# Kernel optimization log

Measured on AMD Instinct MI355X. Metric: run time of the kernel, lower is better.

## Reference

```python
import jax, jax.numpy as jnp
import numpy as np

N_NODES = 50000
N_FEAT = 128
N_EDGES = 1600000
HID = 64


def gcn_conv(x, row, col, w, W, b, n):
    """PyG GCNConv with edge weights and added self-loops (fill_value=1).
    x: [N, Fin]; row/col: [E] (src, dst); w: [E]; W: [Fin, Fout]; b: [Fout].
    """
    loop = jnp.arange(n)
    r = jnp.concatenate([row, loop])
    c = jnp.concatenate([col, loop])
    ww = jnp.concatenate([w, jnp.ones((n,), dtype=x.dtype)])
    deg = jax.ops.segment_sum(ww, c, num_segments=n)  # [N]
    dinv = jnp.where(deg > 0, jax.lax.rsqrt(deg), 0.0)
    norm = dinv[r] * ww * dinv[c]  # [E+N]
    xw = x @ W  # [N, Fout] -- linear before propagate, as in PyG
    msg = norm[:, None] * xw[r]  # gather + scale
    out = jax.ops.segment_sum(msg, c, num_segments=n)  # scatter-add
    return out + b


def setup_inputs() -> dict:
    key = jax.random.key(0)
    ks = jax.random.split(key, 12)
    features = jax.random.normal(ks[0], (N_NODES, N_FEAT), dtype=jnp.float32)
    edge_index = jax.random.randint(ks[1], (2, N_EDGES), 0, N_NODES, dtype=jnp.int64)
    edge_attr = jax.random.uniform(ks[2], (N_EDGES,), dtype=jnp.float32)
    s = 0.05
    # generator encoder: GCNConv(n_feat->64), GCNConv(64->n_feat)
    Wg1 = jax.random.normal(ks[3], (N_FEAT, HID), dtype=jnp.float32) * s
    bg1 = jnp.zeros((HID,), dtype=jnp.float32)
    Wg2 = jax.random.normal(ks[4], (HID, N_FEAT), dtype=jnp.float32) * s
    bg2 = jnp.zeros((N_FEAT,), dtype=jnp.float32)
    # discriminator: GCNConv(n_feat->64), Linear(n_nodes*64 -> 1)
    Wd1 = jax.random.normal(ks[5], (N_FEAT, HID), dtype=jnp.float32) * s
    bd1 = jnp.zeros((HID,), dtype=jnp.float32)
    wfc = jax.random.normal(ks[6], (N_NODES * HID,), dtype=jnp.float32) * 0.001
    bfc = jnp.zeros((), dtype=jnp.float32)
    return {"features": features, "edge_index": edge_index, "edge_attr": edge_attr,
            "Wg1": Wg1, "bg1": bg1, "Wg2": Wg2, "bg2": bg2,
            "Wd1": Wd1, "bd1": bd1, "wfc": wfc, "bfc": bfc}


def reference(features, edge_index, edge_attr, Wg1, bg1, Wg2, bg2, Wd1, bd1, wfc, bfc):
    n = features.shape[0]
    row, col = edge_index[0], edge_index[1]
    # --- generator encoder (eval mode: dropout is a no-op) ---
    h = gcn_conv(features, row, col, edge_attr, Wg1, bg1, n)
    h = jax.nn.relu(h)
    z = jax.nn.sigmoid(gcn_conv(h, row, col, edge_attr, Wg2, bg2, n))  # [N, n_feat]
    # --- GAE inner-product decoder over the given edge list ---
    edge_probs = jax.nn.sigmoid(jnp.sum(z[row] * z[col], axis=-1))  # [E]
    # residual connection
    enc = z + features
    edge_probs = jnp.nan_to_num(edge_probs, nan=0.0)
    # --- discriminator (eval mode: no noise, no dropout) ---
    d = gcn_conv(enc, row, col, edge_probs, Wd1, bd1, n)
    d = jax.nn.relu(d)
    logit = jnp.dot(d.reshape(-1), wfc) + bfc
    return jax.nn.sigmoid(logit)
```

## Files before the change

### kernel.cpp

```cpp
#include <hip/hip_runtime.h>
#include <math.h>

static constexpr int NN = 50000;
static constexpr int NF = 128;
static constexpr int NH = 64;
static constexpr int NE = 1600000;
static constexpr int NBUSED = (NN + 255) / 256;
static constexpr int NWG = 256;
static constexpr int CHUNK = NE / NWG;

typedef unsigned long long u64;
typedef float f32x2 __attribute__((ext_vector_type(2)));


__device__ __forceinline__ float bf2f(unsigned u) { return __uint_as_float(u << 16); }
__device__ __forceinline__ unsigned short f2bf(float f) {
  unsigned b = __float_as_uint(f);
  b += 0x7fffu + ((b >> 16) & 1u);
  return (unsigned short)(b >> 16);
}
__device__ __forceinline__ float sigm(float x) { return 1.f / (1.f + __expf(-x)); }
__device__ __forceinline__ unsigned char f2fp8(float f) {
  int v = __builtin_amdgcn_cvt_pk_fp8_f32(f, f, 0, false);
  return (unsigned char)(v & 0xff);
}
__device__ __forceinline__ void fp8x16_dec(uint4 v, float* o) {
  f32x2 t;
  t = __builtin_amdgcn_cvt_pk_f32_fp8(v.x, false); o[0] = t.x;  o[1] = t.y;
  t = __builtin_amdgcn_cvt_pk_f32_fp8(v.x, true);  o[2] = t.x;  o[3] = t.y;
  t = __builtin_amdgcn_cvt_pk_f32_fp8(v.y, false); o[4] = t.x;  o[5] = t.y;
  t = __builtin_amdgcn_cvt_pk_f32_fp8(v.y, true);  o[6] = t.x;  o[7] = t.y;
  t = __builtin_amdgcn_cvt_pk_f32_fp8(v.z, false); o[8] = t.x;  o[9] = t.y;
  t = __builtin_amdgcn_cvt_pk_f32_fp8(v.z, true);  o[10] = t.x; o[11] = t.y;
  t = __builtin_amdgcn_cvt_pk_f32_fp8(v.w, false); o[12] = t.x; o[13] = t.y;
  t = __builtin_amdgcn_cvt_pk_f32_fp8(v.w, true);  o[14] = t.x; o[15] = t.y;
}
__device__ __forceinline__ uint4 fp8x16_enc(const float* o) {
  uint4 r;
  int v;
  v = __builtin_amdgcn_cvt_pk_fp8_f32(o[0], o[1], 0, false);
  v = __builtin_amdgcn_cvt_pk_fp8_f32(o[2], o[3], v, true);
  r.x = (unsigned)v;
  v = __builtin_amdgcn_cvt_pk_fp8_f32(o[4], o[5], 0, false);
  v = __builtin_amdgcn_cvt_pk_fp8_f32(o[6], o[7], v, true);
  r.y = (unsigned)v;
  v = __builtin_amdgcn_cvt_pk_fp8_f32(o[8], o[9], 0, false);
  v = __builtin_amdgcn_cvt_pk_fp8_f32(o[10], o[11], v, true);
  r.z = (unsigned)v;
  v = __builtin_amdgcn_cvt_pk_fp8_f32(o[12], o[13], 0, false);
  v = __builtin_amdgcn_cvt_pk_fp8_f32(o[14], o[15], v, true);
  r.w = (unsigned)v;
  return r;
}


__global__ __launch_bounds__(256) void bhist_k(const int* __restrict__ col,
                                               int* __restrict__ counts) {
  __shared__ int cnt[256];
  cnt[threadIdx.x] = 0;
  __syncthreads();
  int g = blockIdx.x;
  int e1 = g * CHUNK + CHUNK;
  for (int e = g * CHUNK + threadIdx.x; e < e1; e += 256)
    atomicAdd(&cnt[col[e] >> 8], 1);
  __syncthreads();
  counts[g * 256 + threadIdx.x] = cnt[threadIdx.x];
}

__global__ __launch_bounds__(256) void bscan_k(int* __restrict__ counts) {
  __shared__ int sm[256];
  int b = threadIdx.x;
  int tot = 0;
  for (int g = 0; g < NWG; g++) tot += counts[g * 256 + b];
  sm[b] = tot;
  __syncthreads();
  int v = tot;
  for (int off = 1; off < 256; off <<= 1) {
    int u = (b >= off) ? sm[b - off] : 0;
    __syncthreads();
    sm[b] += u;
    __syncthreads();
  }
  int run = sm[b] - v;
  for (int g = 0; g < NWG; g++) {
    int c = counts[g * 256 + b];
    counts[g * 256 + b] = run;
    run += c;
  }
}

__global__ __launch_bounds__(256) void bpart_k(const int* __restrict__ row,
                                               const int* __restrict__ col,
                                               const float* __restrict__ w,
                                               const int* __restrict__ counts,
                                               u64* __restrict__ ebuf) {
  __shared__ int cur[256];
  int g = blockIdx.x;
  cur[threadIdx.x] = counts[g * 256 + threadIdx.x];
  __syncthreads();
  int e1 = g * CHUNK + CHUNK;
  for (int e = g * CHUNK + threadIdx.x; e < e1; e += 256) {
    int c = col[e];
    int p = atomicAdd(&cur[c >> 8], 1);
    u64 pk = ((u64)(unsigned)__float_as_int(w[e]) << 32) |
             ((unsigned)(c & 255) << 16) | (unsigned)row[e];
    ebuf[p] = pk;
  }
}

__global__ __launch_bounds__(256) void bsortA_k(const u64* __restrict__ ebuf,
                                                const int* __restrict__ counts,
                                                int* __restrict__ rowstart,
                                                float* __restrict__ dinv) {
  __shared__ int cnt[256];
  __shared__ float deg[256];
  __shared__ int sm[256];
  int b = blockIdx.x, t = threadIdx.x;
  cnt[t] = 0;
  deg[t] = 1.0f;
  __syncthreads();
  int boff = counts[b];
  int bend = (b < NBUSED - 1) ? counts[b + 1] : NE;
  for (int e = boff + t; e < bend; e += 256) {
    u64 pk = ebuf[e];
    unsigned lo = (unsigned)pk;
    int c = (lo >> 16) & 255;
    atomicAdd(&cnt[c], 1);
    atomicAdd(&deg[c], __uint_as_float((unsigned)(pk >> 32)));
  }
  __syncthreads();
  int v = cnt[t];
  sm[t] = v;
  __syncthreads();
  for (int off = 1; off < 256; off <<= 1) {
    int u = (t >= off) ? sm[t - off] : 0;
    __syncthreads();
    sm[t] += u;
    __syncthreads();
  }
  int colg = b * 256 + t;
  if (colg < NN) {
    rowstart[colg] = boff + sm[t] - v;
    dinv[colg] = rsqrtf(deg[t]);
  }
  if (b == NBUSED - 1 && t == 0) rowstart[NN] = NE;
}

__global__ __launch_bounds__(256) void bsortB_k(const u64* __restrict__ ebuf,
                                                const int* __restrict__ counts,
                                                const int* __restrict__ rowstart,
                                                const float* __restrict__ dinv,
                                                unsigned* __restrict__ es4) {
  __shared__ int cur[256];
  int b = blockIdx.x, t = threadIdx.x;
  int colg = b * 256 + t;
  cur[t] = (colg < NN) ? rowstart[colg] : NE;
  __syncthreads();
  int boff = counts[b];
  int bend = (b < NBUSED - 1) ? counts[b + 1] : NE;
  for (int e = boff + t; e < bend; e += 256) {
    u64 pk = ebuf[e];
    unsigned lo = (unsigned)pk;
    int r = lo & 0xffff;
    int c = (lo >> 16) & 255;
    float wv = __uint_as_float((unsigned)(pk >> 32));
    int p = atomicAdd(&cur[c], 1);
    es4[p] = ((unsigned)f2bf(dinv[r] * wv) << 16) | (unsigned)r;
  }
}

template<int K, int M, int ACT, bool OUTF, bool OUTH, bool XH, bool OUT8>
__global__ __launch_bounds__(256) void gemm_k(const float* __restrict__ X,
                                              const unsigned short* __restrict__ Xh,
                                              const float* __restrict__ Xadd,
                                              const float* __restrict__ W,
                                              const float* __restrict__ bias,
                                              float* __restrict__ Yf,
                                              unsigned short* __restrict__ Yh,
                                              unsigned char* __restrict__ Y8) {
  __shared__ float Ws[K * M];
  __shared__ float Xs[16][K];
  for (int i = threadIdx.x; i < K * M; i += 256) Ws[i] = W[i];
  int r0 = blockIdx.x * 16;
  for (int i = threadIdx.x; i < 16 * K; i += 256) {
    int r = i / K, k = i % K;
    size_t off = (size_t)(r0 + r) * K + k;
    float v = XH ? bf2f(Xh[off]) : X[off];
    if (Xadd) v += Xadd[off];
    Xs[r][k] = v;
  }
  __syncthreads();
  constexpr int RPT = 16 * M / 256;
  constexpr int RS = 256 / M;
  int colc = threadIdx.x % M;
  int rb = threadIdx.x / M;
  float acc[RPT];
#pragma unroll
  for (int i = 0; i < RPT; i++) acc[i] = 0.f;
  for (int k = 0; k < K; k++) {
    float wv = Ws[k * M + colc];
#pragma unroll
    for (int i = 0; i < RPT; i++) acc[i] += Xs[rb + i * RS][k] * wv;
  }
#pragma unroll
  for (int i = 0; i < RPT; i++) {
    int r = r0 + rb + i * RS;
    float o = acc[i];
    if (ACT > 0) o += bias[colc];
    if (ACT == 2) o = sigm(o);
    if (OUTF) Yf[(size_t)r * M + colc] = o;
    if (OUTH) Yh[(size_t)r * M + colc] = f2bf(o);
    if (OUT8) Y8[(size_t)r * M + colc] = f2fp8(o);
  }
}

template<int MODE>
__global__ __launch_bounds__(256) void agg64_k(const int* __restrict__ rowstart,
                                               const unsigned* __restrict__ es4,
                                               const unsigned char* __restrict__ src8,
                                               const float* __restrict__ dinv,
                                               const float* __restrict__ bias,
                                               unsigned char* __restrict__ out8,
                                               unsigned short* __restrict__ outh,
                                               float* __restrict__ outf,
                                               const float* __restrict__ wfc) {
  int wid = (blockIdx.x * 256 + threadIdx.x) >> 6;
  int lane = threadIdx.x & 63;
  int sub = lane >> 2;
  int l = lane & 3;
  int e0 = rowstart[wid], e1 = rowstart[wid + 1];
  float di = dinv[wid];
  float a[16];
#pragma unroll
  for (int c = 0; c < 16; c++) a[c] = 0.f;
  for (int eb = e0; eb < e1; eb += 32) {
    int eA = eb + sub;
    int eB = eb + 16 + sub;
    bool vA = eA < e1, vB = eB < e1;
    unsigned erA = es4[vA ? eA : e0];
    unsigned erB = es4[vB ? eB : e0];
    int rA = (int)(erA & 0xffffu);
    int rB = (int)(erB & 0xffffu);
    float nmA, nmB;
    if (MODE == 2) {
      nmA = vA ? dinv[rA] * bf2f(erA >> 16) : 0.f;
      nmB = vB ? dinv[rB] * bf2f(erB >> 16) : 0.f;
    } else {
      nmA = vA ? bf2f(erA >> 16) : 0.f;
      nmB = vB ? bf2f(erB >> 16) : 0.f;
    }
    uint4 gA = *(const uint4*)(src8 + (size_t)rA * 64 + l * 16);
    uint4 gB = *(const uint4*)(src8 + (size_t)rB * 64 + l * 16);
    float tA[16], tB[16];
    fp8x16_dec(gA, tA);
    fp8x16_dec(gB, tB);
#pragma unroll
    for (int c = 0; c < 16; c++) a[c] = fmaf(nmA, tA[c], a[c]);
#pragma unroll
    for (int c = 0; c < 16; c++) a[c] = fmaf(nmB, tB[c], a[c]);
  }
#pragma unroll
  for (int c = 0; c < 16; c++) {
    a[c] += __shfl_xor(a[c], 4);
    a[c] += __shfl_xor(a[c], 8);
    a[c] += __shfl_xor(a[c], 16);
    a[c] += __shfl_xor(a[c], 32);
  }
  uint4 sv = *(const uint4*)(src8 + (size_t)wid * 64 + l * 16);
  float sf[16];
  fp8x16_dec(sv, sf);

  if (MODE == 0) {
    if (sub == 0) {
      float o[16];
#pragma unroll
      for (int c4 = 0; c4 < 4; c4++) {
        float4 b4 = *(const float4*)(bias + l * 16 + c4 * 4);
        o[c4 * 4 + 0] = fmaxf(di * (a[c4 * 4 + 0] + di * sf[c4 * 4 + 0]) + b4.x, 0.f);
        o[c4 * 4 + 1] = fmaxf(di * (a[c4 * 4 + 1] + di * sf[c4 * 4 + 1]) + b4.y, 0.f);
        o[c4 * 4 + 2] = fmaxf(di * (a[c4 * 4 + 2] + di * sf[c4 * 4 + 2]) + b4.z, 0.f);
        o[c4 * 4 + 3] = fmaxf(di * (a[c4 * 4 + 3] + di * sf[c4 * 4 + 3]) + b4.w, 0.f);
      }
      *(uint4*)(out8 + (size_t)wid * 64 + l * 16) = fp8x16_enc(o);
    }
  } else if (MODE == 1) {
    if (sub == 0) {
      float o[16];
#pragma unroll
      for (int c = 0; c < 16; c++) o[c] = di * (a[c] + di * sf[c]);
      uint4 p0, p1;
      p0.x = (unsigned)f2bf(o[0]) | ((unsigned)f2bf(o[1]) << 16);
      p0.y = (unsigned)f2bf(o[2]) | ((unsigned)f2bf(o[3]) << 16);
      p0.z = (unsigned)f2bf(o[4]) | ((unsigned)f2bf(o[5]) << 16);
      p0.w = (unsigned)f2bf(o[6]) | ((unsigned)f2bf(o[7]) << 16);
      p1.x = (unsigned)f2bf(o[8]) | ((unsigned)f2bf(o[9]) << 16);
      p1.y = (unsigned)f2bf(o[10]) | ((unsigned)f2bf(o[11]) << 16);
      p1.z = (unsigned)f2bf(o[12]) | ((unsigned)f2bf(o[13]) << 16);
      p1.w = (unsigned)f2bf(o[14]) | ((unsigned)f2bf(o[15]) << 16);
      *(uint4*)(outh + (size_t)wid * 64 + l * 16) = p0;
      *(uint4*)(outh + (size_t)wid * 64 + l * 16 + 8) = p1;
    }
  } else {
    float s = 0.f;
    if (sub == 0) {
#pragma unroll
      for (int c4 = 0; c4 < 4; c4++) {
        float4 b4 = *(const float4*)(bias + l * 16 + c4 * 4);
        float4 w4 = *(const float4*)(wfc + (size_t)wid * 64 + l * 16 + c4 * 4);
        float o0 = fmaxf(di * (a[c4 * 4 + 0] + di * sf[c4 * 4 + 0]) + b4.x, 0.f);
        float o1 = fmaxf(di * (a[c4 * 4 + 1] + di * sf[c4 * 4 + 1]) + b4.y, 0.f);
        float o2 = fmaxf(di * (a[c4 * 4 + 2] + di * sf[c4 * 4 + 2]) + b4.z, 0.f);
        float o3 = fmaxf(di * (a[c4 * 4 + 3] + di * sf[c4 * 4 + 3]) + b4.w, 0.f);
        s += o0 * w4.x + o1 * w4.y + o2 * w4.z + o3 * w4.w;
      }
    }
    s += __shfl_xor(s, 1);
    s += __shfl_xor(s, 2);
    __shared__ float bs[4];
    if (lane == 0) bs[threadIdx.x >> 6] = s;
    __syncthreads();
    if (threadIdx.x == 0) outf[blockIdx.x] = bs[0] + bs[1] + bs[2] + bs[3];
  }
}

__global__ __launch_bounds__(256) void eprob16_k(const int* __restrict__ rowstart,
                                                 unsigned* __restrict__ es4,
                                                 const unsigned char* __restrict__ z8,
                                                 float* __restrict__ dinv2) {
  int wid = (blockIdx.x * 256 + threadIdx.x) >> 6;
  int lane = threadIdx.x & 63;
  int sub = lane >> 3;
  int l = lane & 7;
  uint4 zv = *(const uint4*)(z8 + (size_t)wid * NF + l * 16);
  float zi[16];
  fp8x16_dec(zv, zi);
  int e0 = rowstart[wid], e1 = rowstart[wid + 1];
  float sum = 0.f;
  for (int eb = e0; eb < e1; eb += 16) {
    int eA = eb + sub;
    int eB = eb + 8 + sub;
    bool vA = eA < e1, vB = eB < e1;
    unsigned erA = es4[vA ? eA : e0];
    unsigned erB = es4[vB ? eB : e0];
    int rA = (int)(erA & 0xffffu);
    int rB = (int)(erB & 0xffffu);
    uint4 a4 = *(const uint4*)(z8 + (size_t)rA * NF + l * 16);
    uint4 b4 = *(const uint4*)(z8 + (size_t)rB * NF + l * 16);
    float zr[16];
    fp8x16_dec(a4, zr);
    float dA = 0.f;
#pragma unroll
    for (int c = 0; c < 16; c++) dA = fmaf(zr[c], zi[c], dA);
    fp8x16_dec(b4, zr);
    float dB = 0.f;
#pragma unroll
    for (int c = 0; c < 16; c++) dB = fmaf(zr[c], zi[c], dB);
    dA += __shfl_xor(dA, 1);
    dA += __shfl_xor(dA, 2);
    dA += __shfl_xor(dA, 4);
    dB += __shfl_xor(dB, 1);
    dB += __shfl_xor(dB, 2);
    dB += __shfl_xor(dB, 4);
    if (vA && l == 0) {
      float p = sigm(dA);
      es4[eA] = ((unsigned)f2bf(p) << 16) | (unsigned)rA;
      sum += p;
    }
    if (vB && l == 0) {
      float p = sigm(dB);
      es4[eB] = ((unsigned)f2bf(p) << 16) | (unsigned)rB;
      sum += p;
    }
  }
  sum += __shfl_xor(sum, 8);
  sum += __shfl_xor(sum, 16);
  sum += __shfl_xor(sum, 32);
  if (lane == 0) dinv2[wid] = rsqrtf(1.f + sum);
}

__global__ __launch_bounds__(256) void reduce_k(const float* __restrict__ partials, int n,
                                                const float* __restrict__ bfc,
                                                float* __restrict__ out) {
  float s = 0.f;
  for (int i = threadIdx.x; i < n; i += 256) s += partials[i];
  s += __shfl_xor(s, 1);
  s += __shfl_xor(s, 2);
  s += __shfl_xor(s, 4);
  s += __shfl_xor(s, 8);
  s += __shfl_xor(s, 16);
  s += __shfl_xor(s, 32);
  __shared__ float ws4[4];
  if ((threadIdx.x & 63) == 0) ws4[threadIdx.x >> 6] = s;
  __syncthreads();
  if (threadIdx.x == 0) out[0] = sigm(ws4[0] + ws4[1] + ws4[2] + ws4[3] + bfc[0]);
}


extern "C" void kernel_launch(void* const* d_in, const int* in_sizes, int n_in,
                              void* d_out, int out_size, void* d_ws, size_t ws_size,
                              hipStream_t stream) {
  const float* features = (const float*)d_in[0];
  const int* edge_index = (const int*)d_in[1];
  const float* edge_attr = (const float*)d_in[2];
  const float* Wg1 = (const float*)d_in[3];
  const float* bg1 = (const float*)d_in[4];
  const float* Wg2 = (const float*)d_in[5];
  const float* bg2 = (const float*)d_in[6];
  const float* Wd1 = (const float*)d_in[7];
  const float* bd1 = (const float*)d_in[8];
  const float* wfc = (const float*)d_in[9];
  const float* bfc = (const float*)d_in[10];
  float* out = (float*)d_out;

  const int* row = edge_index;
  const int* col = edge_index + NE;

  char* wsb = (char*)d_ws;
  auto carve = [&](size_t bytes) {
    void* p = wsb;
    wsb += (bytes + 255) & ~(size_t)255;
    return p;
  };
  int*   counts   = (int*)carve((size_t)NWG * 256 * 4);
  int*   rowstart = (int*)carve((NN + 1) * 4);
  float* dinv     = (float*)carve(NN * 4);
  float* dinv2    = (float*)carve(NN * 4);
  u64*   ebuf     = (u64*)carve((size_t)NE * 8);
  unsigned* es4   = (unsigned*)carve((size_t)NE * 4);
  unsigned char* xw8a = (unsigned char*)carve((size_t)NN * NH);
  unsigned char* hh8  = (unsigned char*)carve((size_t)NN * NH);
  unsigned short* ahh = (unsigned short*)carve((size_t)NN * NH * 2);
  unsigned short* zh = (unsigned short*)carve((size_t)NN * NF * 2);
  unsigned char* z8  = (unsigned char*)carve((size_t)NN * NF);
  unsigned char* xw8d = (unsigned char*)carve((size_t)NN * NH);
  float* partials = (float*)carve(12500 * 4);

  const int GG = NN / 16;
  const int GW = NN * 64 / 256;

  bhist_k<<<NWG, 256, 0, stream>>>(col, counts);
  bscan_k<<<1, 256, 0, stream>>>(counts);
  bpart_k<<<NWG, 256, 0, stream>>>(row, col, edge_attr, counts, ebuf);
  bsortA_k<<<NBUSED, 256, 0, stream>>>(ebuf, counts, rowstart, dinv);
  bsortB_k<<<NBUSED, 256, 0, stream>>>(ebuf, counts, rowstart, dinv, es4);

  gemm_k<NF, NH, 0, false, false, false, true><<<GG, 256, 0, stream>>>(
      features, nullptr, nullptr, Wg1, nullptr, nullptr, nullptr, xw8a);
  agg64_k<0><<<GW, 256, 0, stream>>>(rowstart, es4, xw8a, dinv, bg1, hh8, nullptr, nullptr,
                                     nullptr);

  agg64_k<1><<<GW, 256, 0, stream>>>(rowstart, es4, hh8, dinv, nullptr, nullptr, ahh, nullptr,
                                     nullptr);
  gemm_k<NH, NF, 2, false, true, true, true><<<GG, 256, 0, stream>>>(
      nullptr, ahh, nullptr, Wg2, bg2, nullptr, zh, z8);

  eprob16_k<<<GW, 256, 0, stream>>>(rowstart, es4, z8, dinv2);

  gemm_k<NF, NH, 0, false, false, true, true><<<GG, 256, 0, stream>>>(
      nullptr, zh, features, Wd1, nullptr, nullptr, nullptr, xw8d);
  agg64_k<2><<<GW, 256, 0, stream>>>(rowstart, es4, xw8d, dinv2, bd1, nullptr, nullptr,
                                     partials, wfc);

  reduce_k<<<1, 256, 0, stream>>>(partials, GW, bfc, out);
}
```

Baseline: 336.7 us.

## Fuse bucket sort passes and move source-degree scaling into aggregation; add nontemporal hints

Merges the two per-bucket sort kernels into one, so the bucket's ebuf slice is re-read while cached and one launch disappears. Since dinv is no longer ready when edges are written, the stored edge value becomes the raw weight and every aggregation mode multiplies by dinv[row] at gather time, which adds a dependent gather per edge. Nontemporal load/store hints are also added on the streaming edge arrays and the aggregation outputs to reduce cache pollution.

New measurement: 423.1 us. 1.26x slower.

```diff
diff --git a/kernel.cpp b/kernel.cpp
--- a/kernel.cpp
+++ b/kernel.cpp
@@ -11,6 +11,7 @@
 
 typedef unsigned long long u64;
 typedef float f32x2 __attribute__((ext_vector_type(2)));
+typedef unsigned u32x4 __attribute__((ext_vector_type(4)));
 
 
 __device__ __forceinline__ float bf2f(unsigned u) { return __uint_as_float(u << 16); }
@@ -35,8 +36,8 @@
   t = __builtin_amdgcn_cvt_pk_f32_fp8(v.w, false); o[12] = t.x; o[13] = t.y;
   t = __builtin_amdgcn_cvt_pk_f32_fp8(v.w, true);  o[14] = t.x; o[15] = t.y;
 }
-__device__ __forceinline__ uint4 fp8x16_enc(const float* o) {
-  uint4 r;
+__device__ __forceinline__ u32x4 fp8x16_enc(const float* o) {
+  u32x4 r;
   int v;
   v = __builtin_amdgcn_cvt_pk_fp8_f32(o[0], o[1], 0, false);
   v = __builtin_amdgcn_cvt_pk_fp8_f32(o[2], o[3], v, true);
@@ -62,7 +63,7 @@
   int g = blockIdx.x;
   int e1 = g * CHUNK + CHUNK;
   for (int e = g * CHUNK + threadIdx.x; e < e1; e += 256)
-    atomicAdd(&cnt[col[e] >> 8], 1);
+    atomicAdd(&cnt[__builtin_nontemporal_load(&col[e]) >> 8], 1);
   __syncthreads();
   counts[g * 256 + threadIdx.x] = cnt[threadIdx.x];
 }
@@ -100,21 +101,25 @@
   __syncthreads();
   int e1 = g * CHUNK + CHUNK;
   for (int e = g * CHUNK + threadIdx.x; e < e1; e += 256) {
-    int c = col[e];
+    int c = __builtin_nontemporal_load(&col[e]);
+    float wv = __builtin_nontemporal_load(&w[e]);
+    int r = __builtin_nontemporal_load(&row[e]);
     int p = atomicAdd(&cur[c >> 8], 1);
-    u64 pk = ((u64)(unsigned)__float_as_int(w[e]) << 32) |
-             ((unsigned)(c & 255) << 16) | (unsigned)row[e];
-    ebuf[p] = pk;
-  }
-}
-
-__global__ __launch_bounds__(256) void bsortA_k(const u64* __restrict__ ebuf,
-                                                const int* __restrict__ counts,
-                                                int* __restrict__ rowstart,
-                                                float* __restrict__ dinv) {
+    u64 pk = ((u64)(unsigned)__float_as_int(wv) << 32) |
+             ((unsigned)(c & 255) << 16) | (unsigned)r;
+    __builtin_nontemporal_store(pk, &ebuf[p]);
+  }
+}
+
+__global__ __launch_bounds__(256) void bsortAB_k(const u64* __restrict__ ebuf,
+                                                 const int* __restrict__ counts,
+                                                 int* __restrict__ rowstart,
+                                                 float* __restrict__ dinv,
+                                                 unsigned* __restrict__ es4) {
   __shared__ int cnt[256];
   __shared__ float deg[256];
   __shared__ int sm[256];
+  __shared__ int cur[256];
   int b = blockIdx.x, t = threadIdx.x;
   cnt[t] = 0;
   deg[t] = 1.0f;
@@ -138,34 +143,22 @@
     sm[t] += u;
     __syncthreads();
   }
+  int start = boff + sm[t] - v;
+  cur[t] = start;
   int colg = b * 256 + t;
   if (colg < NN) {
-    rowstart[colg] = boff + sm[t] - v;
+    rowstart[colg] = start;
     dinv[colg] = rsqrtf(deg[t]);
   }
   if (b == NBUSED - 1 && t == 0) rowstart[NN] = NE;
-}
-
-__global__ __launch_bounds__(256) void bsortB_k(const u64* __restrict__ ebuf,
-                                                const int* __restrict__ counts,
-                                                const int* __restrict__ rowstart,
-                                                const float* __restrict__ dinv,
-                                                unsigned* __restrict__ es4) {
-  __shared__ int cur[256];
-  int b = blockIdx.x, t = threadIdx.x;
-  int colg = b * 256 + t;
-  cur[t] = (colg < NN) ? rowstart[colg] : NE;
-  __syncthreads();
-  int boff = counts[b];
-  int bend = (b < NBUSED - 1) ? counts[b + 1] : NE;
+  __syncthreads();
   for (int e = boff + t; e < bend; e += 256) {
     u64 pk = ebuf[e];
     unsigned lo = (unsigned)pk;
-    int r = lo & 0xffff;
     int c = (lo >> 16) & 255;
-    float wv = __uint_as_float((unsigned)(pk >> 32));
     int p = atomicAdd(&cur[c], 1);
-    es4[p] = ((unsigned)f2bf(dinv[r] * wv) << 16) | (unsigned)r;
+    unsigned wbf = (unsigned)f2bf(__uint_as_float((unsigned)(pk >> 32)));
+    __builtin_nontemporal_store((wbf << 16) | (lo & 0xffffu), &es4[p]);
   }
 }
 
@@ -237,18 +230,12 @@
     int eA = eb + sub;
     int eB = eb + 16 + sub;
     bool vA = eA < e1, vB = eB < e1;
-    unsigned erA = es4[vA ? eA : e0];
-    unsigned erB = es4[vB ? eB : e0];
+    unsigned erA = __builtin_nontemporal_load(&es4[vA ? eA : e0]);
+    unsigned erB = __builtin_nontemporal_load(&es4[vB ? eB : e0]);
     int rA = (int)(erA & 0xffffu);
     int rB = (int)(erB & 0xffffu);
-    float nmA, nmB;
-    if (MODE == 2) {
-      nmA = vA ? dinv[rA] * bf2f(erA >> 16) : 0.f;
-      nmB = vB ? dinv[rB] * bf2f(erB >> 16) : 0.f;
-    } else {
-      nmA = vA ? bf2f(erA >> 16) : 0.f;
-      nmB = vB ? bf2f(erB >> 16) : 0.f;
-    }
+    float nmA = vA ? dinv[rA] * bf2f(erA >> 16) : 0.f;
+    float nmB = vB ? dinv[rB] * bf2f(erB >> 16) : 0.f;
     uint4 gA = *(const uint4*)(src8 + (size_t)rA * 64 + l * 16);
     uint4 gB = *(const uint4*)(src8 + (size_t)rB * 64 + l * 16);
     float tA[16], tB[16];
@@ -281,14 +268,15 @@
         o[c4 * 4 + 2] = fmaxf(di * (a[c4 * 4 + 2] + di * sf[c4 * 4 + 2]) + b4.z, 0.f);
         o[c4 * 4 + 3] = fmaxf(di * (a[c4 * 4 + 3] + di * sf[c4 * 4 + 3]) + b4.w, 0.f);
       }
-      *(uint4*)(out8 + (size_t)wid * 64 + l * 16) = fp8x16_enc(o);
+      u32x4 p = fp8x16_enc(o);
+      __builtin_nontemporal_store(p, (u32x4*)(out8 + (size_t)wid * 64 + l * 16));
     }
   } else if (MODE == 1) {
     if (sub == 0) {
       float o[16];
 #pragma unroll
       for (int c = 0; c < 16; c++) o[c] = di * (a[c] + di * sf[c]);
-      uint4 p0, p1;
+      u32x4 p0, p1;
       p0.x = (unsigned)f2bf(o[0]) | ((unsigned)f2bf(o[1]) << 16);
       p0.y = (unsigned)f2bf(o[2]) | ((unsigned)f2bf(o[3]) << 16);
       p0.z = (unsigned)f2bf(o[4]) | ((unsigned)f2bf(o[5]) << 16);
@@ -297,8 +285,8 @@
       p1.y = (unsigned)f2bf(o[10]) | ((unsigned)f2bf(o[11]) << 16);
       p1.z = (unsigned)f2bf(o[12]) | ((unsigned)f2bf(o[13]) << 16);
       p1.w = (unsigned)f2bf(o[14]) | ((unsigned)f2bf(o[15]) << 16);
-      *(uint4*)(outh + (size_t)wid * 64 + l * 16) = p0;
-      *(uint4*)(outh + (size_t)wid * 64 + l * 16 + 8) = p1;
+      __builtin_nontemporal_store(p0, (u32x4*)(outh + (size_t)wid * 64 + l * 16));
+      __builtin_nontemporal_store(p1, (u32x4*)(outh + (size_t)wid * 64 + l * 16 + 8));
     }
   } else {
     float s = 0.f;
@@ -340,8 +328,8 @@
     int eA = eb + sub;
     int eB = eb + 8 + sub;
     bool vA = eA < e1, vB = eB < e1;
-    unsigned erA = es4[vA ? eA : e0];
-    unsigned erB = es4[vB ? eB : e0];
+    unsigned erA = __builtin_nontemporal_load(&es4[vA ? eA : e0]);
+    unsigned erB = __builtin_nontemporal_load(&es4[vB ? eB : e0]);
     int rA = (int)(erA & 0xffffu);
     int rB = (int)(erB & 0xffffu);
     uint4 a4 = *(const uint4*)(z8 + (size_t)rA * NF + l * 16);
@@ -363,12 +351,12 @@
     dB += __shfl_xor(dB, 4);
     if (vA && l == 0) {
       float p = sigm(dA);
-      es4[eA] = ((unsigned)f2bf(p) << 16) | (unsigned)rA;
+      __builtin_nontemporal_store(((unsigned)f2bf(p) << 16) | (unsigned)rA, &es4[eA]);
       sum += p;
     }
     if (vB && l == 0) {
       float p = sigm(dB);
-      es4[eB] = ((unsigned)f2bf(p) << 16) | (unsigned)rB;
+      __builtin_nontemporal_store(((unsigned)f2bf(p) << 16) | (unsigned)rB, &es4[eB]);
       sum += p;
     }
   }
@@ -441,8 +429,7 @@
   bhist_k<<<NWG, 256, 0, stream>>>(col, counts);
   bscan_k<<<1, 256, 0, stream>>>(counts);
   bpart_k<<<NWG, 256, 0, stream>>>(row, col, edge_attr, counts, ebuf);
-  bsortA_k<<<NBUSED, 256, 0, stream>>>(ebuf, counts, rowstart, dinv);
-  bsortB_k<<<NBUSED, 256, 0, stream>>>(ebuf, counts, rowstart, dinv, es4);
+  bsortAB_k<<<NBUSED, 256, 0, stream>>>(ebuf, counts, rowstart, dinv, es4);
 
   gemm_k<NF, NH, 0, false, false, false, true><<<GG, 256, 0, stream>>>(
       features, nullptr, nullptr, Wg1, nullptr, nullptr, nullptr, xw8a);
```
